# Kernel tuning notes

Measured on AMD Instinct MI355X. Metric: run time of the kernel, lower is better.

Reference implementation:

```python
import jax, jax.numpy as jnp
import numpy as np

V = 100000
E = 524288
D_IN = 128
D_OUT = 128
NUM_REL = 474
BN_EPS = 1e-5


def setup_inputs() -> dict:
    key = jax.random.key(0)
    ks = jax.random.split(key, 12)
    return {
        "x": jax.random.normal(ks[0], (V, D_IN), dtype=jnp.float32),
        "rel_repr": jax.random.normal(ks[1], (NUM_REL, D_IN), dtype=jnp.float32),
        "edge_norm": jax.random.uniform(ks[2], (E,), dtype=jnp.float32),
        "in_w": jax.random.normal(ks[3], (D_IN, D_OUT), dtype=jnp.float32) * 0.1,
        "out_w": jax.random.normal(ks[4], (D_IN, D_OUT), dtype=jnp.float32) * 0.1,
        "loop_w": jax.random.normal(ks[5], (D_IN, D_OUT), dtype=jnp.float32) * 0.1,
        "w_rel": jax.random.normal(ks[6], (D_IN, D_OUT), dtype=jnp.float32) * 0.1,
        "loop_rel": jax.random.normal(ks[7], (1, D_IN), dtype=jnp.float32),
        "bias": jnp.zeros((D_OUT,), dtype=jnp.float32),
        "src": jax.random.randint(ks[8], (E,), 0, V, dtype=jnp.int32),
        "dst": jax.random.randint(ks[9], (E,), 0, V, dtype=jnp.int32),
        "edge_type": jax.random.randint(ks[10], (E,), 0, NUM_REL, dtype=jnp.int32),
    }


def reference(x, rel_repr, edge_norm, in_w, out_w, loop_w, w_rel, loop_rel, bias, src, dst, edge_type):
    # comp primitive 'mult': edge_data = src_emb * rel[edge_type]   [E, D_IN]
    rel = rel_repr  # num_base=-1 -> rel_wt is None, rel.data = rel_repr
    edge_data = x[src] * rel[edge_type]
    half = edge_data.shape[0] // 2  # static under jit
    # first half of edges -> in_w, second half -> out_w
    msg = jnp.concatenate([edge_data[:half] @ in_w, edge_data[half:] @ out_w], axis=0)
    msg = msg * edge_norm[:, None]
    # agg primitive 'sum': scatter-sum into dst nodes
    agg = jax.ops.segment_sum(msg, dst, num_segments=x.shape[0])  # [V, D_OUT]
    # self-loop path: comp(x, loop_rel) @ loop_w
    loop_msg = (x * loop_rel) @ loop_w
    # comb primitive 'add', scaled by 1/3 (dropout with p=0 is identity)
    h = (agg + loop_msg) * (1.0 / 3.0)
    h = h + bias
    # BatchNorm1d, training-mode batch stats, gamma=1, beta=0
    mean = jnp.mean(h, axis=0)
    var = jnp.mean((h - mean) ** 2, axis=0)
    h = (h - mean) * jax.lax.rsqrt(var + BN_EPS)
    # act primitive 'relu'; ltr=True -> project relations
    return jax.nn.relu(h), rel @ w_rel
```

## Files before the change

kernel.cpp:

```cpp
#include <hip/hip_runtime.h>

#define V 100000
#define VP 100096
#define E_EDGES 524288
#define HALF 262144
#define D 128
#define NREL 474
#define BN_EPS 1e-5f
#define NBLK 98

#define BTP 392
#define ROWTILES 782
#define RED_BLKS 98

#define LDK 392
#define LDB 40

typedef unsigned short u16;
typedef unsigned int u32;
typedef unsigned long long u64;
typedef __attribute__((ext_vector_type(8))) short short8;
typedef __attribute__((ext_vector_type(4))) float f32x4;

__device__ __forceinline__ u16 f2bf(float f) {
    union { float f; u32 u; } v; v.f = f;
    u32 u = v.u;
    return (u16)((u + 0x7fffu + ((u >> 16) & 1u)) >> 16);
}
__device__ __forceinline__ u32 pk2(float a, float b) {
    return (u32)f2bf(a) | ((u32)f2bf(b) << 16);
}

__global__ __launch_bounds__(256) void hist_k(const int* __restrict__ dst, u32* __restrict__ cnt) {
    int e = blockIdx.x * 256 + threadIdx.x;
    if (e >= E_EDGES) return;
    u32 d = (u32)dst[e];
    if (d >= V) d = 0;
    atomicAdd(&cnt[d], 1u);
}

__global__ __launch_bounds__(1024) void scanA_k(const u32* __restrict__ cnt,
                                                u32* __restrict__ cursor,
                                                u32* __restrict__ bsum) {
    __shared__ u32 wsum[16];
    int tid = threadIdx.x, wid = tid >> 6, lane = tid & 63;
    int idx = blockIdx.x * 1024 + tid;
    u32 v = (idx < V) ? cnt[idx] : 0u;
    u32 s = v;
#pragma unroll
    for (int o = 1; o < 64; o <<= 1) {
        u32 t = __shfl_up(s, o, 64);
        if (lane >= o) s += t;
    }
    if (lane == 63) wsum[wid] = s;
    __syncthreads();
    if (wid == 0) {
        u32 wv = (lane < 16) ? wsum[lane] : 0u;
#pragma unroll
        for (int o = 1; o < 16; o <<= 1) {
            u32 t = __shfl_up(wv, o, 64);
            if (lane >= o) wv += t;
        }
        if (lane < 16) wsum[lane] = wv;
    }
    __syncthreads();
    u32 wprev = wid ? wsum[wid - 1] : 0u;
    if (idx < V) cursor[idx] = s + wprev - v;
    if (tid == 0) bsum[blockIdx.x] = wsum[15];
}

__global__ __launch_bounds__(128) void scanB_k(u32* __restrict__ bsum) {
    __shared__ u32 wtot;
    int t = threadIdx.x, lane = t & 63, w = t >> 6;
    u32 v = (t < NBLK) ? bsum[t] : 0u;
    u32 s = v;
#pragma unroll
    for (int o = 1; o < 64; o <<= 1) {
        u32 x = __shfl_up(s, o, 64);
        if (lane >= o) s += x;
    }
    if (w == 0 && lane == 63) wtot = s;
    __syncthreads();
    u32 add = (w == 1) ? wtot : 0u;
    if (t < NBLK) bsum[t] = add + s - v;
}

__global__ __launch_bounds__(1024) void scanC_k(u32* __restrict__ cursor,
                                                const u32* __restrict__ bsum) {
    int idx = blockIdx.x * 1024 + threadIdx.x;
    if (idx < V) cursor[idx] += bsum[blockIdx.x];
}

__global__ __launch_bounds__(256) void fill_rec_k(
    const int* __restrict__ dst, const int* __restrict__ src, const int* __restrict__ etype,
    const float* __restrict__ enorm, u32* __restrict__ cursor, u64* __restrict__ rec) {
    int e = blockIdx.x * 256 + threadIdx.x;
    if (e >= E_EDGES) return;
    u32 d = (u32)dst[e];   if (d >= V) d = 0;
    u32 s = (u32)src[e];   if (s >= V) s = 0;
    u32 t = (u32)etype[e]; if (t >= NREL) t = 0;
    float nm = enorm[e];
    u32 w = s | (t << 17) | ((e < HALF ? 0u : 1u) << 26);
    u32 slot = atomicAdd(&cursor[d], 1u);
    u64 r = (u64)w | ((u64)__float_as_uint(nm) << 32);
    if (slot < E_EDGES) rec[slot] = r;
}

struct Rec { u32 s, t, hf; float nm; };
__device__ __forceinline__ Rec dec(u64 r) {
    Rec q; u32 w = (u32)r;
    q.s = w & 0x1FFFFu;          if (q.s >= V) q.s = 0;
    q.t = (w >> 17) & 0x1FFu;    if (q.t >= NREL) q.t = 0;
    q.hf = (w >> 26) & 1u;
    q.nm = __uint_as_float((u32)(r >> 32));
    return q;
}

__global__ __launch_bounds__(256) void gather_k(
    const float* __restrict__ x, const float* __restrict__ rel,
    const u32* __restrict__ cursor, const u32* __restrict__ cnt,
    const u64* __restrict__ rec, u16* __restrict__ Aagg) {
    int wave = threadIdx.x >> 6, lane = threadIdx.x & 63;
    int v = blockIdx.x * 4 + wave;
    u32* arow = (u32*)(Aagg + (size_t)v * 256);
    if (v >= V) { arow[lane] = 0u; arow[64 + lane] = 0u; return; }

    u32 n = cnt[v], end = cursor[v];
    if (end > E_EDGES) end = E_EDGES;
    if (n > end) n = end;
    u32 p = end - n;
    int col = lane * 2;

    float iA0 = 0.f, iA1 = 0.f, oA0 = 0.f, oA1 = 0.f;
    float iB0 = 0.f, iB1 = 0.f, oB0 = 0.f, oB1 = 0.f;

    for (; p + 4 <= end; p += 4) {
        u64 r0 = rec[p], r1 = rec[p + 1], r2 = rec[p + 2], r3 = rec[p + 3];
        Rec q0 = dec(r0), q1 = dec(r1), q2 = dec(r2), q3 = dec(r3);
        float2 x0 = *(const float2*)(x + (size_t)q0.s * D + col);
        float2 x1 = *(const float2*)(x + (size_t)q1.s * D + col);
        float2 x2 = *(const float2*)(x + (size_t)q2.s * D + col);
        float2 x3 = *(const float2*)(x + (size_t)q3.s * D + col);
        float2 v0 = *(const float2*)(rel + (size_t)q0.t * D + col);
        float2 v1 = *(const float2*)(rel + (size_t)q1.t * D + col);
        float2 v2 = *(const float2*)(rel + (size_t)q2.t * D + col);
        float2 v3 = *(const float2*)(rel + (size_t)q3.t * D + col);
        float f00 = x0.x * v0.x * q0.nm, f01 = x0.y * v0.y * q0.nm;
        float f10 = x1.x * v1.x * q1.nm, f11 = x1.y * v1.y * q1.nm;
        float f20 = x2.x * v2.x * q2.nm, f21 = x2.y * v2.y * q2.nm;
        float f30 = x3.x * v3.x * q3.nm, f31 = x3.y * v3.y * q3.nm;
        if (q0.hf) { oA0 += f00; oA1 += f01; } else { iA0 += f00; iA1 += f01; }
        if (q1.hf) { oB0 += f10; oB1 += f11; } else { iB0 += f10; iB1 += f11; }
        if (q2.hf) { oA0 += f20; oA1 += f21; } else { iA0 += f20; iA1 += f21; }
        if (q3.hf) { oB0 += f30; oB1 += f31; } else { iB0 += f30; iB1 += f31; }
    }
    for (; p < end; p++) {
        u64 r0 = rec[p];
        Rec q0 = dec(r0);
        float2 x0 = *(const float2*)(x + (size_t)q0.s * D + col);
        float2 v0 = *(const float2*)(rel + (size_t)q0.t * D + col);
        float f00 = x0.x * v0.x * q0.nm, f01 = x0.y * v0.y * q0.nm;
        if (q0.hf) { oA0 += f00; oA1 += f01; } else { iA0 += f00; iA1 += f01; }
    }
    float a0 = iA0 + iB0, a1 = iA1 + iB1;
    float b0 = oA0 + oB0, b1 = oA1 + oB1;
    arow[lane]      = pk2(a0, a1);
    arow[64 + lane] = pk2(b0, b1);
}

__global__ __launch_bounds__(128) void bt_k(
    const float* __restrict__ in_w, const float* __restrict__ out_w,
    const float* __restrict__ loop_w, u16* __restrict__ Bt) {
    int n = blockIdx.x;
    int t = threadIdx.x;
    const float* Ws[3] = {in_w, out_w, loop_w};
#pragma unroll
    for (int seg = 0; seg < 3; seg++)
        Bt[(size_t)n * BTP + seg * 128 + t] = f2bf(Ws[seg][(size_t)t * D + n]);
    if (t < BTP - 384) Bt[(size_t)n * BTP + 384 + t] = 0;
}

__global__ __launch_bounds__(512, 4) void gemm_k(
    const u16* __restrict__ Aagg, const u16* __restrict__ Bt,
    const float* __restrict__ x, const float* __restrict__ loop_rel,
    float* __restrict__ h_out, float* __restrict__ psum, float* __restrict__ psq) {
    __shared__ u16 Bs[64 * BTP];
    __shared__ float s_sum[64], s_sq[64];
    int tid = threadIdx.x, wave = tid >> 6, lane = tid & 63;
    int half = blockIdx.x & 1;
    int rt   = blockIdx.x >> 1;
    int row0 = rt * 128;

    if (tid < 64) s_sum[tid] = 0.f;
    else if (tid < 128) s_sq[tid - 64] = 0.f;

    {
        const u16* srcB = Bt + (size_t)half * 64 * BTP;
#pragma unroll
        for (int it = 0; it < 7; it++) {
            int c = it * 512 + tid;
            if (c < 3136) *(short8*)(Bs + (size_t)c * 8) = *(const short8*)(srcB + (size_t)c * 8);
        }
    }
    __syncthreads();

    int m16 = lane & 15;
    int kq = (lane >> 4) * 8;
    int gvm = row0 + wave * 16 + m16;
    const u16* arow = Aagg + (size_t)gvm * 256;

    f32x4 acc[4];
#pragma unroll
    for (int ct = 0; ct < 4; ct++) acc[ct] = (f32x4){0.f, 0.f, 0.f, 0.f};

#pragma unroll
    for (int ks = 0; ks < 8; ks++) {
        short8 a = *(const short8*)(arow + ks * 32 + kq);
#pragma unroll
        for (int ct = 0; ct < 4; ct++) {
            short8 b = *(const short8*)(Bs + (size_t)(ct * 16 + m16) * BTP + ks * 32 + kq);
            acc[ct] = __builtin_amdgcn_mfma_f32_16x16x32_bf16(a, b, acc[ct], 0, 0, 0);
        }
    }
#pragma unroll
    for (int kk = 0; kk < 4; kk++) {
        short8 a = (short8){0, 0, 0, 0, 0, 0, 0, 0};
        if (gvm < V) {
            const float* xp = x + (size_t)gvm * D + kk * 32 + kq;
            const float* lp = loop_rel + kk * 32 + kq;
            float4 x0 = *(const float4*)xp, x1 = *(const float4*)(xp + 4);
            float4 l0 = *(const float4*)lp, l1 = *(const float4*)(lp + 4);
            union { u32 u[4]; short8 s; } c;
            c.u[0] = pk2(x0.x * l0.x, x0.y * l0.y);
            c.u[1] = pk2(x0.z * l0.z, x0.w * l0.w);
            c.u[2] = pk2(x1.x * l1.x, x1.y * l1.y);
            c.u[3] = pk2(x1.z * l1.z, x1.w * l1.w);
            a = c.s;
        }
#pragma unroll
        for (int ct = 0; ct < 4; ct++) {
            short8 b = *(const short8*)(Bs + (size_t)(ct * 16 + m16) * BTP + 256 + kk * 32 + kq);
            acc[ct] = __builtin_amdgcn_mfma_f32_16x16x32_bf16(a, b, acc[ct], 0, 0, 0);
        }
    }

    int m4 = (lane >> 4) * 4;
#pragma unroll
    for (int ct = 0; ct < 4; ct++) {
        float ls = 0.f, lq = 0.f;
#pragma unroll
        for (int i = 0; i < 4; i++) {
            int gv = row0 + wave * 16 + m4 + i;
            if (gv < V) {
                float h = acc[ct][i] * (1.0f / 3.0f);
                h_out[(size_t)gv * D + half * 64 + ct * 16 + m16] = h;
                ls += h; lq += h * h;
            }
        }
        atomicAdd(&s_sum[ct * 16 + m16], ls);
        atomicAdd(&s_sq[ct * 16 + m16], lq);
    }
    __syncthreads();
    if (tid < 64) psum[(size_t)rt * 128 + half * 64 + tid] = s_sum[tid];
    else if (tid < 128) psq[(size_t)rt * 128 + half * 64 + (tid - 64)] = s_sq[tid - 64];
}

__global__ __launch_bounds__(256) void bn_reduce(
    const float* __restrict__ psum, const float* __restrict__ psq,
    float* __restrict__ colsum, float* __restrict__ colsumsq) {
    int t = threadIdx.x;
    int c = t & 127;
    const float* srcp = (t < 128) ? psum : psq;
    float s = 0.f;
    int r0 = blockIdx.x * 8;
#pragma unroll
    for (int i = 0; i < 8; i++) {
        int r = r0 + i;
        if (r < ROWTILES) s += srcp[(size_t)r * 128 + c];
    }
    atomicAdd(((t < 128) ? colsum : colsumsq) + c, s);
}

__global__ void bn_finalize(const float* __restrict__ colsum, const float* __restrict__ colsumsq,
                            float* __restrict__ mean, float* __restrict__ scale) {
    int t = threadIdx.x;
    float m = colsum[t] * (1.0f / (float)V);
    if (!isfinite(m)) m = 0.f;
    float var = colsumsq[t] * (1.0f / (float)V) - m * m;
    if (!isfinite(var) || var < 0.f) var = 0.f;
    mean[t] = m;
    scale[t] = rsqrtf(var + BN_EPS);
}

__global__ __launch_bounds__(256) void bn_relu(
    float* __restrict__ hio, const float* __restrict__ mean, const float* __restrict__ scale) {
    int idx = (blockIdx.x * 256 + threadIdx.x) * 4;
    if (idx >= V * D) return;
    int col = idx & (D - 1);
    float4 hv = *(const float4*)(hio + idx);
    float f0 = (hv.x - mean[col + 0]) * scale[col + 0];
    float f1 = (hv.y - mean[col + 1]) * scale[col + 1];
    float f2 = (hv.z - mean[col + 2]) * scale[col + 2];
    float f3 = (hv.w - mean[col + 3]) * scale[col + 3];
    f0 = (f0 > 0.f) ? f0 : 0.f;
    f1 = (f1 > 0.f) ? f1 : 0.f;
    f2 = (f2 > 0.f) ? f2 : 0.f;
    f3 = (f3 > 0.f) ? f3 : 0.f;
    float4 ov; ov.x = f0; ov.y = f1; ov.z = f2; ov.w = f3;
    *(float4*)(hio + idx) = ov;
}

__global__ __launch_bounds__(128) void rel_gemm(
    const float* __restrict__ rel, const float* __restrict__ w, float* __restrict__ out1) {
    __shared__ float rs[D];
    int t = threadIdx.x;
    int r = blockIdx.x;
    rs[t] = rel[(size_t)r * D + t];
    __syncthreads();
    float s = 0.f;
#pragma unroll 8
    for (int k = 0; k < D; k++) s += rs[k] * w[(size_t)k * D + t];
    out1[(size_t)r * D + t] = s;
}

__global__ __launch_bounds__(1024) void scan_k(const u32* __restrict__ cnt,
                                               u32* __restrict__ cursor) {
    __shared__ u32 wsum[16];
    __shared__ u32 carry_s;
    int tid = threadIdx.x, wid = tid >> 6, lane = tid & 63;
    if (tid == 0) carry_s = 0;
    __syncthreads();
    for (int base = 0; base < V; base += 1024) {
        int idx = base + tid;
        u32 v = (idx < V) ? cnt[idx] : 0u;
        u32 s = v;
#pragma unroll
        for (int o = 1; o < 64; o <<= 1) {
            u32 t = __shfl_up(s, o, 64);
            if (lane >= o) s += t;
        }
        if (lane == 63) wsum[wid] = s;
        __syncthreads();
        if (wid == 0) {
            u32 wv = (lane < 16) ? wsum[lane] : 0u;
#pragma unroll
            for (int o = 1; o < 16; o <<= 1) {
                u32 t = __shfl_up(wv, o, 64);
                if (lane >= o) wv += t;
            }
            if (lane < 16) wsum[lane] = wv;
        }
        __syncthreads();
        u32 wprev = (wid == 0) ? 0u : wsum[wid - 1];
        u32 c = carry_s;
        if (idx < V) cursor[idx] = c + s + wprev - v;
        u32 tot = wsum[15];
        __syncthreads();
        if (tid == 0) carry_s = c + tot;
        __syncthreads();
    }
}

__global__ __launch_bounds__(256) void fill_k(
    const int* __restrict__ dst, u32* __restrict__ cursor, u32* __restrict__ eid) {
    int e = blockIdx.x * 256 + threadIdx.x;
    if (e >= E_EDGES) return;
    u32 d = (u32)dst[e];
    if (d >= V) d = 0;
    u32 slot = atomicAdd(&cursor[d], 1u);
    if (slot < E_EDGES) eid[slot] = (u32)e;
}

__global__ __launch_bounds__(256, 1) void fused_k(
    const float* __restrict__ x, const float* __restrict__ rel, const float* __restrict__ loop_rel,
    const float* __restrict__ in_w, const float* __restrict__ out_w, const float* __restrict__ loop_w,
    const float* __restrict__ enorm,
    const int* __restrict__ src, const int* __restrict__ etype,
    const u32* __restrict__ cursor, const u32* __restrict__ cnt,
    const u32* __restrict__ eid,
    float* __restrict__ h_out, float* __restrict__ colsum, float* __restrict__ colsumsq) {
    __shared__ u16 Alds[64 * LDK];
    __shared__ u16 Bs[D * LDB];
    __shared__ float s_sum[D], s_sq[D];

    int tid = threadIdx.x, wave = tid >> 6, lane = tid & 63;
    int row0 = blockIdx.x * 64;

    if (tid < D) { s_sum[tid] = 0.f; s_sq[tid] = 0.f; }

    for (int i = 0; i < 16; i++) {
        int row = wave * 16 + i;
        int gv = row0 + row;
        u32* arow = (u32*)(Alds + row * LDK);
        if (gv < V) {
            float a0 = 0.f, a1 = 0.f, b0 = 0.f, b1 = 0.f;
            float c0 = 0.f, c1 = 0.f, d0 = 0.f, d1 = 0.f;
            u32 n = cnt[gv];
            u32 end = cursor[gv];
            u32 beg = (end >= n) ? end - n : 0u;
            if (beg >= E_EDGES) { beg = 0; n = 0; }
            if (n > E_EDGES - beg) n = E_EDGES - beg;
            u32 nend = beg + n;
            u32 p = beg;
            for (; p + 2 <= nend; p += 2) {
                u32 e0 = eid[p];           if (e0 >= E_EDGES) e0 = 0;
                u32 e1 = eid[p + 1];       if (e1 >= E_EDGES) e1 = 0;
                u32 s0 = (u32)src[e0];     if (s0 >= V) s0 = 0;
                u32 s1 = (u32)src[e1];     if (s1 >= V) s1 = 0;
                u32 t0 = (u32)etype[e0];   if (t0 >= NREL) t0 = 0;
                u32 t1 = (u32)etype[e1];   if (t1 >= NREL) t1 = 0;
                float n0 = enorm[e0];
                float n1 = enorm[e1];
                float2 xv0 = *(const float2*)(x + (size_t)s0 * D + lane * 2);
                float2 xv1 = *(const float2*)(x + (size_t)s1 * D + lane * 2);
                float2 rv0 = *(const float2*)(rel + (size_t)t0 * D + lane * 2);
                float2 rv1 = *(const float2*)(rel + (size_t)t1 * D + lane * 2);
                float f00 = xv0.x * rv0.x * n0, f01 = xv0.y * rv0.y * n0;
                float f10 = xv1.x * rv1.x * n1, f11 = xv1.y * rv1.y * n1;
                if (e0 < HALF) { a0 += f00; a1 += f01; } else { b0 += f00; b1 += f01; }
                if (e1 < HALF) { c0 += f10; c1 += f11; } else { d0 += f10; d1 += f11; }
            }
            if (p < nend) {
                u32 e0 = eid[p];           if (e0 >= E_EDGES) e0 = 0;
                u32 s0 = (u32)src[e0];     if (s0 >= V) s0 = 0;
                u32 t0 = (u32)etype[e0];   if (t0 >= NREL) t0 = 0;
                float n0 = enorm[e0];
                float2 xv0 = *(const float2*)(x + (size_t)s0 * D + lane * 2);
                float2 rv0 = *(const float2*)(rel + (size_t)t0 * D + lane * 2);
                float f00 = xv0.x * rv0.x * n0, f01 = xv0.y * rv0.y * n0;
                if (e0 < HALF) { a0 += f00; a1 += f01; } else { b0 += f00; b1 += f01; }
            }
            a0 += c0; a1 += c1; b0 += d0; b1 += d1;
            float2 xv = *(const float2*)(x + (size_t)gv * D + lane * 2);
            float2 lv = *(const float2*)(loop_rel + lane * 2);
            arow[lane]       = pk2(a0, a1);
            arow[64 + lane]  = pk2(b0, b1);
            arow[128 + lane] = pk2(xv.x * lv.x, xv.y * lv.y);
        } else {
            arow[lane] = 0u; arow[64 + lane] = 0u; arow[128 + lane] = 0u;
        }
    }
    __syncthreads();

    f32x4 acc[8];
#pragma unroll
    for (int ct = 0; ct < 8; ct++) acc[ct] = (f32x4){0.f, 0.f, 0.f, 0.f};

    int m = wave * 16 + (lane & 15);
    int kq = (lane >> 4) * 8;
    int bk = tid >> 3;
    int bn0 = (tid & 7) * 16;

    for (int ks = 0; ks < 12; ks++) {
        int k0 = ks * 32;
        int seg = k0 >> 7;
        int kloc = k0 & 127;
        const float* W = (seg == 0) ? in_w : (seg == 1 ? out_w : loop_w);
#pragma unroll
        for (int j = 0; j < 16; j += 2) {
            float2 w2 = *(const float2*)(W + (size_t)(kloc + bk) * D + bn0 + j);
            Bs[(bn0 + j) * LDB + bk]     = f2bf(w2.x);
            Bs[(bn0 + j + 1) * LDB + bk] = f2bf(w2.y);
        }
        __syncthreads();
        short8 a = *(const short8*)(Alds + m * LDK + k0 + kq);
#pragma unroll
        for (int ct = 0; ct < 8; ct++) {
            short8 b = *(const short8*)(Bs + (ct * 16 + (lane & 15)) * LDB + kq);
            acc[ct] = __builtin_amdgcn_mfma_f32_16x16x32_bf16(a, b, acc[ct], 0, 0, 0);
        }
        __syncthreads();
    }

    int m4 = (lane >> 4) * 4;
#pragma unroll
    for (int ct = 0; ct < 8; ct++) {
        float ls = 0.f, lq = 0.f;
#pragma unroll
        for (int i = 0; i < 4; i++) {
            int gv = row0 + wave * 16 + m4 + i;
            if (gv < V) {
                float h = acc[ct][i] * (1.0f / 3.0f);
                h_out[(size_t)gv * D + ct * 16 + (lane & 15)] = h;
                ls += h; lq += h * h;
            }
        }
        atomicAdd(&s_sum[ct * 16 + (lane & 15)], ls);
        atomicAdd(&s_sq[ct * 16 + (lane & 15)], lq);
    }
    __syncthreads();
    if (tid < D) atomicAdd(&colsum[tid], s_sum[tid]);
    else atomicAdd(&colsumsq[tid - D], s_sq[tid - D]);
}

extern "C" void kernel_launch(void* const* d_in, const int* in_sizes, int n_in,
                              void* d_out, int out_size, void* d_ws, size_t ws_size,
                              hipStream_t stream) {
    const float* x        = (const float*)d_in[0];
    const float* rel_repr = (const float*)d_in[1];
    const float* enorm    = (const float*)d_in[2];
    const float* in_w     = (const float*)d_in[3];
    const float* out_w    = (const float*)d_in[4];
    const float* loop_w   = (const float*)d_in[5];
    const float* w_rel    = (const float*)d_in[6];
    const float* loop_rel = (const float*)d_in[7];
    const int* src   = (const int*)d_in[9];
    const int* dst   = (const int*)d_in[10];
    const int* etype = (const int*)d_in[11];

    float* out0 = (float*)d_out;
    float* out1 = (float*)d_out + (size_t)V * D;

    char* ws = (char*)d_ws;

    {
        size_t off = 0;
        u32* cnt        = (u32*)(ws + off); off += (size_t)V * 4;
        float* colsum   = (float*)(ws + off); off += 512;
        float* colsumsq = (float*)(ws + off); off += 512;
        size_t zero_bytes = off;
        u32* cursor = (u32*)(ws + off); off += (size_t)V * 4;
        float* meanp  = (float*)(ws + off); off += 512;
        float* scalep = (float*)(ws + off); off += 512;
        u32* bsum   = (u32*)(ws + off); off += 512;
        u16* Bt     = (u16*)(ws + off); off += (size_t)128 * BTP * 2;
        float* psum = (float*)(ws + off); off += (size_t)ROWTILES * 128 * 4;
        float* psq  = (float*)(ws + off); off += (size_t)ROWTILES * 128 * 4;
        u64* rec    = (u64*)(ws + off); off += (size_t)E_EDGES * 8;
        u16* Aagg   = (u16*)(ws + off); off += (size_t)VP * 256 * 2;

        if (ws_size >= off) {
            hipMemsetAsync(d_ws, 0, zero_bytes, stream);
            bt_k<<<128, 128, 0, stream>>>(in_w, out_w, loop_w, Bt);
            hist_k<<<(E_EDGES + 255) / 256, 256, 0, stream>>>(dst, cnt);
            scanA_k<<<NBLK, 1024, 0, stream>>>(cnt, cursor, bsum);
            scanB_k<<<1, 128, 0, stream>>>(bsum);
            scanC_k<<<NBLK, 1024, 0, stream>>>(cursor, bsum);
            fill_rec_k<<<(E_EDGES + 255) / 256, 256, 0, stream>>>(dst, src, etype, enorm, cursor, rec);
            gather_k<<<VP / 4, 256, 0, stream>>>(x, rel_repr, cursor, cnt, rec, Aagg);
            gemm_k<<<ROWTILES * 2, 512, 0, stream>>>(Aagg, Bt, x, loop_rel, out0, psum, psq);
            bn_reduce<<<RED_BLKS, 256, 0, stream>>>(psum, psq, colsum, colsumsq);
            bn_finalize<<<1, 128, 0, stream>>>(colsum, colsumsq, meanp, scalep);
            bn_relu<<<(V * D / 4 + 255) / 256, 256, 0, stream>>>(out0, meanp, scalep);
            rel_gemm<<<NREL, 128, 0, stream>>>(rel_repr, w_rel, out1);
            return;
        }
    }

    {
        size_t off = 0;
        u32* cnt      = (u32*)(ws + off); off += (size_t)V * 4;
        float* colsum = (float*)(ws + off); off += 512;
        float* colsumsq = (float*)(ws + off); off += 512;
        size_t zero_bytes = off;
        u32* cursor   = (u32*)(ws + off); off += (size_t)V * 4;
        float* meanp  = (float*)(ws + off); off += 512;
        float* scalep = (float*)(ws + off); off += 512;
        u32* eid      = (u32*)(ws + off); off += (size_t)E_EDGES * 4;

        if (ws_size < off) return;

        hipMemsetAsync(d_ws, 0, zero_bytes, stream);
        hist_k<<<(E_EDGES + 255) / 256, 256, 0, stream>>>(dst, cnt);
        scan_k<<<1, 1024, 0, stream>>>(cnt, cursor);
        fill_k<<<(E_EDGES + 255) / 256, 256, 0, stream>>>(dst, cursor, eid);
        fused_k<<<(V + 63) / 64, 256, 0, stream>>>(x, rel_repr, loop_rel, in_w, out_w, loop_w,
                                                   enorm, src, etype,
                                                   cursor, cnt, eid,
                                                   out0, colsum, colsumsq);
        bn_finalize<<<1, 128, 0, stream>>>(colsum, colsumsq, meanp, scalep);
        bn_relu<<<(V * D / 4 + 255) / 256, 256, 0, stream>>>(out0, meanp, scalep);
        rel_gemm<<<NREL, 128, 0, stream>>>(rel_repr, w_rel, out1);
    }
}
```

Baseline: 332.7 us.

## Fold scan offset into consumers, prefetch edge records, swizzle LDS, fuse BN and rel GEMM

Removes the scanC kernel by adding the per-block prefix offset directly in fill_rec and gather. The gather loop now software-prefetches the next four edge records, replacing the separate tail loop. The GEMM drops LDS padding in favour of an XOR swizzle, issues its A-fragment and x loads before the B tile is staged to overlap latency, and drops the occupancy hint from the launch bounds. BN finalize, BN+ReLU and the relation GEMM merge into one kernel, recomputing mean and scale per element, to cut launch count at the cost of some redundant arithmetic.

```diff
diff --git a/kernel.cpp b/kernel.cpp
--- a/kernel.cpp
+++ b/kernel.cpp
@@ -9,9 +9,10 @@
 #define BN_EPS 1e-5f
 #define NBLK 98
 
-#define BTP 392
 #define ROWTILES 782
 #define RED_BLKS 98
+#define RELB 237
+#define BNBLK 12500
 
 #define LDK 392
 #define LDB 40
@@ -85,15 +86,10 @@
     if (t < NBLK) bsum[t] = add + s - v;
 }
 
-__global__ __launch_bounds__(1024) void scanC_k(u32* __restrict__ cursor,
-                                                const u32* __restrict__ bsum) {
-    int idx = blockIdx.x * 1024 + threadIdx.x;
-    if (idx < V) cursor[idx] += bsum[blockIdx.x];
-}
-
 __global__ __launch_bounds__(256) void fill_rec_k(
     const int* __restrict__ dst, const int* __restrict__ src, const int* __restrict__ etype,
-    const float* __restrict__ enorm, u32* __restrict__ cursor, u64* __restrict__ rec) {
+    const float* __restrict__ enorm, u32* __restrict__ cursor, const u32* __restrict__ bsum,
+    u64* __restrict__ rec) {
     int e = blockIdx.x * 256 + threadIdx.x;
     if (e >= E_EDGES) return;
     u32 d = (u32)dst[e];   if (d >= V) d = 0;
@@ -101,7 +97,7 @@
     u32 t = (u32)etype[e]; if (t >= NREL) t = 0;
     float nm = enorm[e];
     u32 w = s | (t << 17) | ((e < HALF ? 0u : 1u) << 26);
-    u32 slot = atomicAdd(&cursor[d], 1u);
+    u32 slot = atomicAdd(&cursor[d], 1u) + bsum[d >> 10];
     u64 r = (u64)w | ((u64)__float_as_uint(nm) << 32);
     if (slot < E_EDGES) rec[slot] = r;
 }
@@ -119,13 +115,15 @@
 __global__ __launch_bounds__(256) void gather_k(
     const float* __restrict__ x, const float* __restrict__ rel,
     const u32* __restrict__ cursor, const u32* __restrict__ cnt,
-    const u64* __restrict__ rec, u16* __restrict__ Aagg) {
+    const u32* __restrict__ bsum, const u64* __restrict__ rec, u16* __restrict__ Aagg) {
     int wave = threadIdx.x >> 6, lane = threadIdx.x & 63;
     int v = blockIdx.x * 4 + wave;
+    if (v >= VP) return;
     u32* arow = (u32*)(Aagg + (size_t)v * 256);
     if (v >= V) { arow[lane] = 0u; arow[64 + lane] = 0u; return; }
 
-    u32 n = cnt[v], end = cursor[v];
+    u32 n = cnt[v];
+    u32 end = cursor[v] + bsum[v >> 10];
     if (end > E_EDGES) end = E_EDGES;
     if (n > end) n = end;
     u32 p = end - n;
@@ -134,9 +132,20 @@
     float iA0 = 0.f, iA1 = 0.f, oA0 = 0.f, oA1 = 0.f;
     float iB0 = 0.f, iB1 = 0.f, oB0 = 0.f, oB1 = 0.f;
 
-    for (; p + 4 <= end; p += 4) {
-        u64 r0 = rec[p], r1 = rec[p + 1], r2 = rec[p + 2], r3 = rec[p + 3];
-        Rec q0 = dec(r0), q1 = dec(r1), q2 = dec(r2), q3 = dec(r3);
+    u64 rb0 = 0, rb1 = 0, rb2 = 0, rb3 = 0;
+    if (p     < end) rb0 = rec[p];
+    if (p + 1 < end) rb1 = rec[p + 1];
+    if (p + 2 < end) rb2 = rec[p + 2];
+    if (p + 3 < end) rb3 = rec[p + 3];
+
+    for (u32 q = p; q < end; q += 4) {
+        u64 rn0 = 0, rn1 = 0, rn2 = 0, rn3 = 0;
+        if (q + 4 < end) rn0 = rec[q + 4];
+        if (q + 5 < end) rn1 = rec[q + 5];
+        if (q + 6 < end) rn2 = rec[q + 6];
+        if (q + 7 < end) rn3 = rec[q + 7];
+
+        Rec q0 = dec(rb0), q1 = dec(rb1), q2 = dec(rb2), q3 = dec(rb3);
         float2 x0 = *(const float2*)(x + (size_t)q0.s * D + col);
         float2 x1 = *(const float2*)(x + (size_t)q1.s * D + col);
         float2 x2 = *(const float2*)(x + (size_t)q2.s * D + col);
@@ -153,19 +162,11 @@
         if (q1.hf) { oB0 += f10; oB1 += f11; } else { iB0 += f10; iB1 += f11; }
         if (q2.hf) { oA0 += f20; oA1 += f21; } else { iA0 += f20; iA1 += f21; }
         if (q3.hf) { oB0 += f30; oB1 += f31; } else { iB0 += f30; iB1 += f31; }
-    }
-    for (; p < end; p++) {
-        u64 r0 = rec[p];
-        Rec q0 = dec(r0);
-        float2 x0 = *(const float2*)(x + (size_t)q0.s * D + col);
-        float2 v0 = *(const float2*)(rel + (size_t)q0.t * D + col);
-        float f00 = x0.x * v0.x * q0.nm, f01 = x0.y * v0.y * q0.nm;
-        if (q0.hf) { oA0 += f00; oA1 += f01; } else { iA0 += f00; iA1 += f01; }
-    }
-    float a0 = iA0 + iB0, a1 = iA1 + iB1;
-    float b0 = oA0 + oB0, b1 = oA1 + oB1;
-    arow[lane]      = pk2(a0, a1);
-    arow[64 + lane] = pk2(b0, b1);
+
+        rb0 = rn0; rb1 = rn1; rb2 = rn2; rb3 = rn3;
+    }
+    arow[lane]      = pk2(iA0 + iB0, iA1 + iB1);
+    arow[64 + lane] = pk2(oA0 + oB0, oA1 + oB1);
 }
 
 __global__ __launch_bounds__(128) void bt_k(
@@ -176,15 +177,14 @@
     const float* Ws[3] = {in_w, out_w, loop_w};
 #pragma unroll
     for (int seg = 0; seg < 3; seg++)
-        Bt[(size_t)n * BTP + seg * 128 + t] = f2bf(Ws[seg][(size_t)t * D + n]);
-    if (t < BTP - 384) Bt[(size_t)n * BTP + 384 + t] = 0;
-}
-
-__global__ __launch_bounds__(512, 4) void gemm_k(
+        Bt[(size_t)n * 384 + seg * 128 + t] = f2bf(Ws[seg][(size_t)t * D + n]);
+}
+
+__global__ __launch_bounds__(512) void gemm_k(
     const u16* __restrict__ Aagg, const u16* __restrict__ Bt,
     const float* __restrict__ x, const float* __restrict__ loop_rel,
     float* __restrict__ h_out, float* __restrict__ psum, float* __restrict__ psq) {
-    __shared__ u16 Bs[64 * BTP];
+    __shared__ u16 Bs[64 * 384];
     __shared__ float s_sum[64], s_sq[64];
     int tid = threadIdx.x, wave = tid >> 6, lane = tid & 63;
     int half = blockIdx.x & 1;
@@ -194,53 +194,67 @@
     if (tid < 64) s_sum[tid] = 0.f;
     else if (tid < 128) s_sq[tid - 64] = 0.f;
 
-    {
-        const u16* srcB = Bt + (size_t)half * 64 * BTP;
-#pragma unroll
-        for (int it = 0; it < 7; it++) {
-            int c = it * 512 + tid;
-            if (c < 3136) *(short8*)(Bs + (size_t)c * 8) = *(const short8*)(srcB + (size_t)c * 8);
-        }
-    }
-    __syncthreads();
-
     int m16 = lane & 15;
     int kq = (lane >> 4) * 8;
     int gvm = row0 + wave * 16 + m16;
     const u16* arow = Aagg + (size_t)gvm * 256;
-
+    bool vok = gvm < V;
+
+    short8 af[8];
+#pragma unroll
+    for (int ks = 0; ks < 8; ks++) af[ks] = *(const short8*)(arow + ks * 32 + kq);
+    float4 xf[8];
+    {
+        const float* xp = x + (size_t)gvm * D + kq;
+#pragma unroll
+        for (int kk = 0; kk < 4; kk++) {
+            xf[2 * kk]     = vok ? *(const float4*)(xp + kk * 32)     : (float4){0.f, 0.f, 0.f, 0.f};
+            xf[2 * kk + 1] = vok ? *(const float4*)(xp + kk * 32 + 4) : (float4){0.f, 0.f, 0.f, 0.f};
+        }
+    }
+
+    {
+        const u16* srcB = Bt + (size_t)half * 64 * 384;
+        char* bsb = (char*)Bs;
+#pragma unroll
+        for (int it = 0; it < 6; it++) {
+            int c = it * 512 + tid;
+            int n = c / 48, s = c - n * 48;
+            short8 vv = *(const short8*)(srcB + (size_t)n * 384 + s * 8);
+            *(short8*)(bsb + (((u32)(n * 768 + s * 16)) ^ (u32)((n & 7) << 4))) = vv;
+        }
+    }
+    __syncthreads();
+
+    const char* bsb = (const char*)Bs;
     f32x4 acc[4];
 #pragma unroll
     for (int ct = 0; ct < 4; ct++) acc[ct] = (f32x4){0.f, 0.f, 0.f, 0.f};
 
 #pragma unroll
     for (int ks = 0; ks < 8; ks++) {
-        short8 a = *(const short8*)(arow + ks * 32 + kq);
 #pragma unroll
         for (int ct = 0; ct < 4; ct++) {
-            short8 b = *(const short8*)(Bs + (size_t)(ct * 16 + m16) * BTP + ks * 32 + kq);
-            acc[ct] = __builtin_amdgcn_mfma_f32_16x16x32_bf16(a, b, acc[ct], 0, 0, 0);
+            int n = ct * 16 + m16;
+            short8 b = *(const short8*)(bsb + (((u32)(n * 768 + (ks * 32 + kq) * 2)) ^ (u32)((n & 7) << 4)));
+            acc[ct] = __builtin_amdgcn_mfma_f32_16x16x32_bf16(af[ks], b, acc[ct], 0, 0, 0);
         }
     }
 #pragma unroll
     for (int kk = 0; kk < 4; kk++) {
-        short8 a = (short8){0, 0, 0, 0, 0, 0, 0, 0};
-        if (gvm < V) {
-            const float* xp = x + (size_t)gvm * D + kk * 32 + kq;
-            const float* lp = loop_rel + kk * 32 + kq;
-            float4 x0 = *(const float4*)xp, x1 = *(const float4*)(xp + 4);
-            float4 l0 = *(const float4*)lp, l1 = *(const float4*)(lp + 4);
-            union { u32 u[4]; short8 s; } c;
-            c.u[0] = pk2(x0.x * l0.x, x0.y * l0.y);
-            c.u[1] = pk2(x0.z * l0.z, x0.w * l0.w);
-            c.u[2] = pk2(x1.x * l1.x, x1.y * l1.y);
-            c.u[3] = pk2(x1.z * l1.z, x1.w * l1.w);
-            a = c.s;
-        }
+        float4 l0 = *(const float4*)(loop_rel + kk * 32 + kq);
+        float4 l1 = *(const float4*)(loop_rel + kk * 32 + kq + 4);
+        float4 x0 = xf[2 * kk], x1 = xf[2 * kk + 1];
+        union { u32 u[4]; short8 s; } c;
+        c.u[0] = pk2(x0.x * l0.x, x0.y * l0.y);
+        c.u[1] = pk2(x0.z * l0.z, x0.w * l0.w);
+        c.u[2] = pk2(x1.x * l1.x, x1.y * l1.y);
+        c.u[3] = pk2(x1.z * l1.z, x1.w * l1.w);
 #pragma unroll
         for (int ct = 0; ct < 4; ct++) {
-            short8 b = *(const short8*)(Bs + (size_t)(ct * 16 + m16) * BTP + 256 + kk * 32 + kq);
-            acc[ct] = __builtin_amdgcn_mfma_f32_16x16x32_bf16(a, b, acc[ct], 0, 0, 0);
+            int n = ct * 16 + m16;
+            short8 b = *(const short8*)(bsb + (((u32)(n * 768 + (256 + kk * 32 + kq) * 2)) ^ (u32)((n & 7) << 4)));
+            acc[ct] = __builtin_amdgcn_mfma_f32_16x16x32_bf16(c.s, b, acc[ct], 0, 0, 0);
         }
     }
 
@@ -281,46 +295,54 @@
     atomicAdd(((t < 128) ? colsum : colsumsq) + c, s);
 }
 
-__global__ void bn_finalize(const float* __restrict__ colsum, const float* __restrict__ colsumsq,
-                            float* __restrict__ mean, float* __restrict__ scale) {
-    int t = threadIdx.x;
-    float m = colsum[t] * (1.0f / (float)V);
-    if (!isfinite(m)) m = 0.f;
-    float var = colsumsq[t] * (1.0f / (float)V) - m * m;
-    if (!isfinite(var) || var < 0.f) var = 0.f;
-    mean[t] = m;
-    scale[t] = rsqrtf(var + BN_EPS);
-}
-
-__global__ __launch_bounds__(256) void bn_relu(
-    float* __restrict__ hio, const float* __restrict__ mean, const float* __restrict__ scale) {
-    int idx = (blockIdx.x * 256 + threadIdx.x) * 4;
+__global__ __launch_bounds__(256) void final_k(
+    float* __restrict__ hio, const float* __restrict__ colsum, const float* __restrict__ colsumsq,
+    const float* __restrict__ rel, const float* __restrict__ w, float* __restrict__ out1) {
+    int bid = blockIdx.x;
+    if (bid < RELB) {
+        __shared__ float rs[2][D];
+        int rh = threadIdx.x >> 7, c = threadIdx.x & 127;
+        int r = bid * 2 + rh;
+        rs[rh][c] = rel[(size_t)r * D + c];
+        __syncthreads();
+        float s = 0.f;
+#pragma unroll 8
+        for (int k = 0; k < D; k++) s += rs[rh][k] * w[(size_t)k * D + c];
+        out1[(size_t)r * D + c] = s;
+        return;
+    }
+    int idx = ((bid - RELB) * 256 + threadIdx.x) * 4;
     if (idx >= V * D) return;
     int col = idx & (D - 1);
     float4 hv = *(const float4*)(hio + idx);
-    float f0 = (hv.x - mean[col + 0]) * scale[col + 0];
-    float f1 = (hv.y - mean[col + 1]) * scale[col + 1];
-    float f2 = (hv.z - mean[col + 2]) * scale[col + 2];
-    float f3 = (hv.w - mean[col + 3]) * scale[col + 3];
-    f0 = (f0 > 0.f) ? f0 : 0.f;
-    f1 = (f1 > 0.f) ? f1 : 0.f;
-    f2 = (f2 > 0.f) ? f2 : 0.f;
-    f3 = (f3 > 0.f) ? f3 : 0.f;
-    float4 ov; ov.x = f0; ov.y = f1; ov.z = f2; ov.w = f3;
+    float4 ov;
+    {
+        float m0 = colsum[col + 0] * (1.0f / (float)V);
+        float m1 = colsum[col + 1] * (1.0f / (float)V);
+        float m2 = colsum[col + 2] * (1.0f / (float)V);
+        float m3 = colsum[col + 3] * (1.0f / (float)V);
+        if (!isfinite(m0)) m0 = 0.f;
+        if (!isfinite(m1)) m1 = 0.f;
+        if (!isfinite(m2)) m2 = 0.f;
+        if (!isfinite(m3)) m3 = 0.f;
+        float v0 = colsumsq[col + 0] * (1.0f / (float)V) - m0 * m0;
+        float v1 = colsumsq[col + 1] * (1.0f / (float)V) - m1 * m1;
+        float v2 = colsumsq[col + 2] * (1.0f / (float)V) - m2 * m2;
+        float v3 = colsumsq[col + 3] * (1.0f / (float)V) - m3 * m3;
+        if (!isfinite(v0) || v0 < 0.f) v0 = 0.f;
+        if (!isfinite(v1) || v1 < 0.f) v1 = 0.f;
+        if (!isfinite(v2) || v2 < 0.f) v2 = 0.f;
+        if (!isfinite(v3) || v3 < 0.f) v3 = 0.f;
+        float f0 = (hv.x - m0) * rsqrtf(v0 + BN_EPS);
+        float f1 = (hv.y - m1) * rsqrtf(v1 + BN_EPS);
+        float f2 = (hv.z - m2) * rsqrtf(v2 + BN_EPS);
+        float f3 = (hv.w - m3) * rsqrtf(v3 + BN_EPS);
+        ov.x = (f0 > 0.f) ? f0 : 0.f;
+        ov.y = (f1 > 0.f) ? f1 : 0.f;
+        ov.z = (f2 > 0.f) ? f2 : 0.f;
+        ov.w = (f3 > 0.f) ? f3 : 0.f;
+    }
     *(float4*)(hio + idx) = ov;
-}
-
-__global__ __launch_bounds__(128) void rel_gemm(
-    const float* __restrict__ rel, const float* __restrict__ w, float* __restrict__ out1) {
-    __shared__ float rs[D];
-    int t = threadIdx.x;
-    int r = blockIdx.x;
-    rs[t] = rel[(size_t)r * D + t];
-    __syncthreads();
-    float s = 0.f;
-#pragma unroll 8
-    for (int k = 0; k < D; k++) s += rs[k] * w[(size_t)k * D + t];
-    out1[(size_t)r * D + t] = s;
 }
 
 __global__ __launch_bounds__(1024) void scan_k(const u32* __restrict__ cnt,
@@ -493,6 +515,48 @@
     else atomicAdd(&colsumsq[tid - D], s_sq[tid - D]);
 }
 
+__global__ void bn_finalize(const float* __restrict__ colsum, const float* __restrict__ colsumsq,
+                            float* __restrict__ mean, float* __restrict__ scale) {
+    int t = threadIdx.x;
+    float m = colsum[t] * (1.0f / (float)V);
+    if (!isfinite(m)) m = 0.f;
+    float var = colsumsq[t] * (1.0f / (float)V) - m * m;
+    if (!isfinite(var) || var < 0.f) var = 0.f;
+    mean[t] = m;
+    scale[t] = rsqrtf(var + BN_EPS);
+}
+
+__global__ __launch_bounds__(256) void bn_relu(
+    float* __restrict__ hio, const float* __restrict__ mean, const float* __restrict__ scale) {
+    int idx = (blockIdx.x * 256 + threadIdx.x) * 4;
+    if (idx >= V * D) return;
+    int col = idx & (D - 1);
+    float4 hv = *(const float4*)(hio + idx);
+    float f0 = (hv.x - mean[col + 0]) * scale[col + 0];
+    float f1 = (hv.y - mean[col + 1]) * scale[col + 1];
+    float f2 = (hv.z - mean[col + 2]) * scale[col + 2];
+    float f3 = (hv.w - mean[col + 3]) * scale[col + 3];
+    f0 = (f0 > 0.f) ? f0 : 0.f;
+    f1 = (f1 > 0.f) ? f1 : 0.f;
+    f2 = (f2 > 0.f) ? f2 : 0.f;
+    f3 = (f3 > 0.f) ? f3 : 0.f;
+    float4 ov; ov.x = f0; ov.y = f1; ov.z = f2; ov.w = f3;
+    *(float4*)(hio + idx) = ov;
+}
+
+__global__ __launch_bounds__(128) void rel_gemm(
+    const float* __restrict__ rel, const float* __restrict__ w, float* __restrict__ out1) {
+    __shared__ float rs[D];
+    int t = threadIdx.x;
+    int r = blockIdx.x;
+    rs[t] = rel[(size_t)r * D + t];
+    __syncthreads();
+    float s = 0.f;
+#pragma unroll 8
+    for (int k = 0; k < D; k++) s += rs[k] * w[(size_t)k * D + t];
+    out1[(size_t)r * D + t] = s;
+}
+
 extern "C" void kernel_launch(void* const* d_in, const int* in_sizes, int n_in,
                               void* d_out, int out_size, void* d_ws, size_t ws_size,
                               hipStream_t stream) {
@@ -520,10 +584,8 @@
         float* colsumsq = (float*)(ws + off); off += 512;
         size_t zero_bytes = off;
         u32* cursor = (u32*)(ws + off); off += (size_t)V * 4;
-        float* meanp  = (float*)(ws + off); off += 512;
-        float* scalep = (float*)(ws + off); off += 512;
         u32* bsum   = (u32*)(ws + off); off += 512;
-        u16* Bt     = (u16*)(ws + off); off += (size_t)128 * BTP * 2;
+        u16* Bt     = (u16*)(ws + off); off += (size_t)128 * 384 * 2;
         float* psum = (float*)(ws + off); off += (size_t)ROWTILES * 128 * 4;
         float* psq  = (float*)(ws + off); off += (size_t)ROWTILES * 128 * 4;
         u64* rec    = (u64*)(ws + off); off += (size_t)E_EDGES * 8;
@@ -535,14 +597,11 @@
             hist_k<<<(E_EDGES + 255) / 256, 256, 0, stream>>>(dst, cnt);
             scanA_k<<<NBLK, 1024, 0, stream>>>(cnt, cursor, bsum);
             scanB_k<<<1, 128, 0, stream>>>(bsum);
-            scanC_k<<<NBLK, 1024, 0, stream>>>(cursor, bsum);
-            fill_rec_k<<<(E_EDGES + 255) / 256, 256, 0, stream>>>(dst, src, etype, enorm, cursor, rec);
-            gather_k<<<VP / 4, 256, 0, stream>>>(x, rel_repr, cursor, cnt, rec, Aagg);
+            fill_rec_k<<<(E_EDGES + 255) / 256, 256, 0, stream>>>(dst, src, etype, enorm, cursor, bsum, rec);
+            gather_k<<<VP / 4, 256, 0, stream>>>(x, rel_repr, cursor, cnt, bsum, rec, Aagg);
             gemm_k<<<ROWTILES * 2, 512, 0, stream>>>(Aagg, Bt, x, loop_rel, out0, psum, psq);
             bn_reduce<<<RED_BLKS, 256, 0, stream>>>(psum, psq, colsum, colsumsq);
-            bn_finalize<<<1, 128, 0, stream>>>(colsum, colsumsq, meanp, scalep);
-            bn_relu<<<(V * D / 4 + 255) / 256, 256, 0, stream>>>(out0, meanp, scalep);
-            rel_gemm<<<NREL, 128, 0, stream>>>(rel_repr, w_rel, out1);
+            final_k<<<RELB + BNBLK, 256, 0, stream>>>(out0, colsum, colsumsq, rel_repr, w_rel, out1);
             return;
         }
     }
```

Result: no change. 335.1 us (+0.7%).
